# Kernel optimization log

Measured on AMD Instinct MI355X. Metric: run time of the kernel, lower is better.

## Reference

```python
import jax, jax.numpy as jnp
import numpy as np

N_NODES = 50000
N_EDGES = 800000
D = 128
N_LAYERS = 3
EPS = 1e-5  # torch LayerNorm default


def _gcn_conv(x, src, dst, dinv, W, b):
    # PyG GCNConv: h = x @ W; out[i] = sum_{(s->i)} dinv[s]*dinv[i]*h[s] + dinv[i]^2*h[i] + b
    h = x @ W
    norm = dinv[src] * dinv[dst]                      # [E]
    msgs = h[src] * norm[:, None]                     # [E, D] gather
    agg = jax.ops.segment_sum(msgs, dst, num_segments=N_NODES)  # scatter-add
    agg = agg + h * (dinv * dinv)[:, None]            # self-loop term
    return agg + b


def _layer_norm(x, gamma, beta):
    mu = jnp.mean(x, axis=-1, keepdims=True)
    var = jnp.mean(jnp.square(x - mu), axis=-1, keepdims=True)
    return (x - mu) * jax.lax.rsqrt(var + EPS) * gamma + beta


def setup_inputs() -> dict:
    key = jax.random.key(0)
    ks = jax.random.split(key, 4)
    x = jax.random.normal(ks[0], (N_NODES, D), dtype=jnp.float32)
    edge_index = jax.random.randint(ks[1], (2, N_EDGES), 0, N_NODES, dtype=jnp.int64)
    Ws = jax.random.normal(ks[2], (N_LAYERS, D, D), dtype=jnp.float32) * (1.0 / np.sqrt(D))
    bs = jnp.zeros((N_LAYERS, D), dtype=jnp.float32)
    gammas = jnp.ones((N_LAYERS, D), dtype=jnp.float32)
    betas = jnp.zeros((N_LAYERS, D), dtype=jnp.float32)
    return {"x": x, "edge_index": edge_index, "Ws": Ws, "bs": bs,
            "gammas": gammas, "betas": betas}


def reference(x, edge_index, Ws, bs, gammas, betas):
    src, dst = edge_index[0], edge_index[1]
    # GCN symmetric normalization with self-loops: deg[i] = in-degree(i) + 1
    deg = jnp.zeros((N_NODES,), dtype=x.dtype).at[dst].add(1.0) + 1.0
    dinv = jax.lax.rsqrt(deg)
    h = x
    for i in range(N_LAYERS):
        x_new = _gcn_conv(h, src, dst, dinv, Ws[i], bs[i])
        x_new = _layer_norm(x_new, gammas[i], betas[i])
        x_new = jax.nn.relu(x_new)  # dropout is identity in eval mode
        h = h + x_new if i > 0 else x_new
    return h
```

## Files before the change

kernel.cpp:

```cpp
#include <hip/hip_runtime.h>
#include <hip/hip_bf16.h>

#define NN 50000
#define NE 800000
#define DD 128
#define NB 196
#define NSB 49
#define PH (64 * NB)
#define FS 1024
#define NSL 782
#define HHB NSL
#define QB 3125
#define WB 192
#define LG 3125
#define LN_EPS 1e-5f

typedef __bf16 bf16x8 __attribute__((ext_vector_type(8)));
typedef float f32x4 __attribute__((ext_vector_type(4)));

__device__ inline ushort f2bf_bits(float f) {
    union { __hip_bfloat16 h; ushort u; } c;
    c.h = __float2bfloat16(f);
    return c.u;
}

__device__ inline void accum_q16(float* acc, uint4 v, float ww) {
    uint q0 = v.x, q1 = v.y, q2 = v.z, q3 = v.w;
    acc[0]  = fmaf(ww, (float)(char)(q0), acc[0]);
    acc[1]  = fmaf(ww, (float)(char)(q0 >> 8), acc[1]);
    acc[2]  = fmaf(ww, (float)(char)(q0 >> 16), acc[2]);
    acc[3]  = fmaf(ww, (float)(char)(q0 >> 24), acc[3]);
    acc[4]  = fmaf(ww, (float)(char)(q1), acc[4]);
    acc[5]  = fmaf(ww, (float)(char)(q1 >> 8), acc[5]);
    acc[6]  = fmaf(ww, (float)(char)(q1 >> 16), acc[6]);
    acc[7]  = fmaf(ww, (float)(char)(q1 >> 24), acc[7]);
    acc[8]  = fmaf(ww, (float)(char)(q2), acc[8]);
    acc[9]  = fmaf(ww, (float)(char)(q2 >> 8), acc[9]);
    acc[10] = fmaf(ww, (float)(char)(q2 >> 16), acc[10]);
    acc[11] = fmaf(ww, (float)(char)(q2 >> 24), acc[11]);
    acc[12] = fmaf(ww, (float)(char)(q3), acc[12]);
    acc[13] = fmaf(ww, (float)(char)(q3 >> 8), acc[13]);
    acc[14] = fmaf(ww, (float)(char)(q3 >> 16), acc[14]);
    acc[15] = fmaf(ww, (float)(char)(q3 >> 24), acc[15]);
}

__global__ void hist_cast_kernel(const int* __restrict__ dst, int* __restrict__ counts,
                                 int* __restrict__ rank, const float* __restrict__ x,
                                 uint2* __restrict__ qf0, float* __restrict__ sc0,
                                 const float* __restrict__ W, ushort* __restrict__ Wt) {
    int b = blockIdx.x;
    if (b < HHB) {
        int base = b * FS;
#pragma unroll 4
        for (int i = threadIdx.x; i < FS; i += 256) {
            int e = base + i;
            if (e < NE) rank[e] = atomicAdd(&counts[dst[e]], 1);
        }
    } else if (b < HHB + QB) {
        int bb = b - HHB;
        int group = threadIdx.x >> 4, t = threadIdx.x & 15;
        int node = bb * 16 + group;
        const float4* xr = (const float4*)(x + (size_t)node * DD + t * 8);
        float4 v0 = xr[0], v1 = xr[1];
        float vals[8] = {v0.x, v0.y, v0.z, v0.w, v1.x, v1.y, v1.z, v1.w};
        float am = 0.f;
#pragma unroll
        for (int i = 0; i < 8; ++i) am = fmaxf(am, fabsf(vals[i]));
#pragma unroll
        for (int off = 1; off <= 8; off <<= 1) am = fmaxf(am, __shfl_xor(am, off, 64));
        float inv = 127.f / fmaxf(am, 1e-20f);
        uint lo = 0, hi = 0;
#pragma unroll
        for (int i = 0; i < 4; ++i) {
            int q = __float2int_rn(vals[i] * inv);
            lo |= ((uint)(q & 0xff)) << (8 * i);
        }
#pragma unroll
        for (int i = 0; i < 4; ++i) {
            int q = __float2int_rn(vals[4 + i] * inv);
            hi |= ((uint)(q & 0xff)) << (8 * i);
        }
        uint2 pk; pk.x = lo; pk.y = hi;
        qf0[node * 16 + t] = pk;
        if (t == 0) sc0[node] = am / 127.f;
    } else {
        int i = (b - HHB - QB) * 256 + threadIdx.x;
        int l = i >> 14, k = (i >> 7) & 127, n = i & 127;
        Wt[l * 16384 + n * 128 + k] = f2bf_bits(W[i]);
    }
}

__global__ __launch_bounds__(1024) void scan1024_blocks(int* __restrict__ data,
                                                        int* __restrict__ bsums) {
    __shared__ int ws[16];
    int gid = blockIdx.x * 1024 + threadIdx.x;
    int lane = threadIdx.x & 63, wid = threadIdx.x >> 6;
    int v = (gid < NN) ? data[gid] : 0;
    int x = v;
#pragma unroll
    for (int off = 1; off < 64; off <<= 1) {
        int t = __shfl_up(x, off, 64);
        if (lane >= off) x += t;
    }
    if (lane == 63) ws[wid] = x;
    __syncthreads();
    if (threadIdx.x == 0) {
        int run = 0;
        for (int i = 0; i < 16; ++i) { int t = ws[i]; ws[i] = run; run += t; }
        bsums[blockIdx.x] = run;
    }
    __syncthreads();
    if (gid < NN) data[gid] = x - v + ws[wid];
}

__global__ __launch_bounds__(1024) void scan_sums1024(int* __restrict__ bsums, int nb) {
    __shared__ int ws[16];
    int tid = threadIdx.x;
    int lane = tid & 63, wid = tid >> 6;
    int v = (tid < nb) ? bsums[tid] : 0;
    int x = v;
#pragma unroll
    for (int off = 1; off < 64; off <<= 1) {
        int t = __shfl_up(x, off, 64);
        if (lane >= off) x += t;
    }
    if (lane == 63) ws[wid] = x;
    __syncthreads();
    if (tid == 0) {
        int run = 0;
        for (int i = 0; i < 16; ++i) { int t = ws[i]; ws[i] = run; run += t; }
    }
    __syncthreads();
    if (tid < nb) bsums[tid] = x - v + ws[wid];
}

__global__ void finalize_kernel(const int* __restrict__ excl, const int* __restrict__ bsums,
                                int* __restrict__ row_ptr, float* __restrict__ dinv,
                                int* __restrict__ degarr, int* __restrict__ bh) {
    __shared__ int lh[64];
    if (threadIdx.x < 64) lh[threadIdx.x] = 0;
    __syncthreads();
    int d = blockIdx.x * 256 + threadIdx.x;
    if (d < NN) {
        int p0 = excl[d] + bsums[d >> 10];
        int nxt = (d == NN - 1) ? NE : excl[d + 1] + bsums[(d + 1) >> 10];
        int deg = nxt - p0;
        row_ptr[d] = p0;
        dinv[d] = rsqrtf((float)deg + 1.0f);
        degarr[d] = deg;
        atomicAdd(&lh[63 - min(deg, 63)], 1);
    }
    __syncthreads();
    if (threadIdx.x < 64) bh[threadIdx.x * NB + blockIdx.x] = lh[threadIdx.x];
    if (blockIdx.x == 0 && threadIdx.x == 0) row_ptr[NN] = NE;
}

__global__ __launch_bounds__(1024) void permscan_kernel(int* __restrict__ bh) {
    __shared__ int wsum[16];
    const int CH = 13;
    int tid = threadIdx.x;
    int base = tid * CH;
    int vals[CH];
    int s = 0;
#pragma unroll
    for (int i = 0; i < CH; ++i) {
        int idx = base + i;
        int v = (idx < PH) ? bh[idx] : 0;
        vals[i] = s;
        s += v;
    }
    int lane = tid & 63, wid = tid >> 6;
    int x = s;
#pragma unroll
    for (int off = 1; off < 64; off <<= 1) {
        int t = __shfl_up(x, off, 64);
        if (lane >= off) x += t;
    }
    if (lane == 63) wsum[wid] = x;
    __syncthreads();
    if (tid == 0) {
        int run = 0;
        for (int i = 0; i < 16; ++i) { int t = wsum[i]; wsum[i] = run; run += t; }
    }
    __syncthreads();
    int texcl = x - s + wsum[wid];
#pragma unroll
    for (int i = 0; i < CH; ++i) {
        int idx = base + i;
        if (idx < PH) bh[idx] = texcl + vals[i];
    }
}

__global__ void scatter_fill_kernel(const int* __restrict__ degarr, const int* __restrict__ bh,
                                    int* __restrict__ perm, const int* __restrict__ src,
                                    const int* __restrict__ dst, const int* __restrict__ excl,
                                    const int* __restrict__ bsums, const int* __restrict__ rank,
                                    const float* __restrict__ dinv, int2* __restrict__ edge2) {
    if (blockIdx.x < NB) {
        __shared__ int lh[64];
        __shared__ int lbase[64];
        if (threadIdx.x < 64) {
            lh[threadIdx.x] = 0;
            lbase[threadIdx.x] = bh[threadIdx.x * NB + blockIdx.x];
        }
        __syncthreads();
        int gid = blockIdx.x * 256 + threadIdx.x;
        if (gid < NN) {
            int b = 63 - min(degarr[gid], 63);
            int r = atomicAdd(&lh[b], 1);
            perm[lbase[b] + r] = gid;
        }
    } else {
        int bb = blockIdx.x - NB;
        if (bb == 0 && threadIdx.x < 8) {
            int2 z; z.x = 0; z.y = 0;
            edge2[NE + threadIdx.x] = z;
        }
        int base = bb * FS;
#pragma unroll 4
        for (int i = threadIdx.x; i < FS; i += 256) {
            int e = base + i;
            if (e < NE) {
                int d = dst[e];
                int s = src[e];
                int pos = excl[d] + bsums[d >> 10] + rank[e];
                int2 o;
                o.x = s;
                o.y = __float_as_int(dinv[s] * dinv[d]);
                edge2[pos] = o;
            }
        }
    }
}

template <bool RES, bool FINAL>
__global__ __launch_bounds__(128) void layer_kernel(
    const uint4* __restrict__ qin, const float* __restrict__ scin,
    const ushort* __restrict__ fin, const int* __restrict__ row_ptr,
    const int2* __restrict__ edge2, const int* __restrict__ perm,
    const float* __restrict__ dinv, const ushort* __restrict__ Wt,
    const float* __restrict__ bias, const float* __restrict__ gamma,
    const float* __restrict__ beta, ushort* __restrict__ fout, char* __restrict__ qfout,
    float* __restrict__ scout, float* __restrict__ out) {
    __shared__ uint4 sA[16 * 17];
    __shared__ int sNode[16];
    __shared__ float sLN1[2][16], sLN2[2][16];
    __shared__ float sMX[2][16];

    int tid = threadIdx.x;
    int wv = tid >> 6, lane = tid & 63;
    int grp = lane >> 3, ln = lane & 7;
    int arow = wv * 8 + grp;
    int slot = blockIdx.x * 16 + arow;
    int node = perm[slot];
    if (ln == 0) sNode[arow] = node;

    {
        int beg = row_ptr[node], deg = row_ptr[node + 1] - beg;
        int nbt = (deg + 7) >> 3;
        float acc[16] = {};

        uint4 qself = qin[node * 8 + ln];
        float wself = dinv[node];
        wself = wself * wself * scin[node];

        const int2* eb = edge2 + beg;
        int bsel = lane & 56;
        for (int b = 0; b < nbt; ++b) {
            int lim = deg - b * 8;
            int2 a = eb[b * 8 + ln];
            float wf = __int_as_float(a.y) * scin[a.x];
            int sj[8];
            float W8[8];
#pragma unroll
            for (int j = 0; j < 8; ++j) sj[j] = __shfl(a.x, bsel + j, 64);
#pragma unroll
            for (int j = 0; j < 8; ++j) W8[j] = __shfl(wf, bsel + j, 64);
            uint4 Q[8];
#pragma unroll
            for (int j = 0; j < 8; ++j) Q[j] = qin[sj[j] * 8 + ln];
#pragma unroll
            for (int j = 0; j < 8; ++j) accum_q16(acc, Q[j], (j < lim) ? W8[j] : 0.f);
        }
        accum_q16(acc, qself, wself);

        union { ushort us[16]; uint4 u[2]; } pk;
#pragma unroll
        for (int i = 0; i < 16; ++i) pk.us[i] = f2bf_bits(acc[i]);
        sA[arow * 17 + 2 * ln] = pk.u[0];
        sA[arow * 17 + 2 * ln + 1] = pk.u[1];
    }
    __syncthreads();

    int q4 = lane >> 4, m = lane & 15;
    f32x4 c0 = (f32x4){0.f, 0.f, 0.f, 0.f};
    f32x4 c1 = c0, c2 = c0, c3 = c0;
    int ncb = 64 * wv;
#pragma unroll
    for (int kk = 0; kk < 4; ++kk) {
        bf16x8 af = *(const bf16x8*)&sA[m * 17 + kk * 4 + q4];
        const ushort* wb = Wt + (size_t)(ncb + m) * DD + kk * 32 + q4 * 8;
        c0 = __builtin_amdgcn_mfma_f32_16x16x32_bf16(af, *(const bf16x8*)(wb), c0, 0, 0, 0);
        c1 = __builtin_amdgcn_mfma_f32_16x16x32_bf16(af, *(const bf16x8*)(wb + 16 * DD), c1, 0, 0, 0);
        c2 = __builtin_amdgcn_mfma_f32_16x16x32_bf16(af, *(const bf16x8*)(wb + 32 * DD), c2, 0, 0, 0);
        c3 = __builtin_amdgcn_mfma_f32_16x16x32_bf16(af, *(const bf16x8*)(wb + 48 * DD), c3, 0, 0, 0);
    }

    float bb0 = bias[ncb + m], bb1 = bias[ncb + 16 + m];
    float bb2 = bias[ncb + 32 + m], bb3 = bias[ncb + 48 + m];
    float s1[4], s2[4];
#pragma unroll
    for (int r = 0; r < 4; ++r) {
        float v0 = c0[r] + bb0, v1 = c1[r] + bb1, v2 = c2[r] + bb2, v3 = c3[r] + bb3;
        c0[r] = v0; c1[r] = v1; c2[r] = v2; c3[r] = v3;
        s1[r] = (v0 + v1) + (v2 + v3);
        s2[r] = (v0 * v0 + v1 * v1) + (v2 * v2 + v3 * v3);
    }
#pragma unroll
    for (int off = 1; off <= 8; off <<= 1) {
#pragma unroll
        for (int r = 0; r < 4; ++r) {
            s1[r] += __shfl_xor(s1[r], off, 64);
            s2[r] += __shfl_xor(s2[r], off, 64);
        }
    }
    if (m == 0) {
#pragma unroll
        for (int r = 0; r < 4; ++r) {
            sLN1[wv][q4 * 4 + r] = s1[r];
            sLN2[wv][q4 * 4 + r] = s2[r];
        }
    }
    __syncthreads();
    float ga0 = gamma[ncb + m], ga1 = gamma[ncb + 16 + m];
    float ga2 = gamma[ncb + 32 + m], ga3 = gamma[ncb + 48 + m];
    float be0 = beta[ncb + m], be1 = beta[ncb + 16 + m];
    float be2 = beta[ncb + 32 + m], be3 = beta[ncb + 48 + m];
    float o0v[4], o1v[4], o2v[4], o3v[4], rmax[4];
#pragma unroll
    for (int r = 0; r < 4; ++r) {
        int row = q4 * 4 + r;
        float S1 = sLN1[0][row] + sLN1[1][row];
        float S2 = sLN2[0][row] + sLN2[1][row];
        float mu = S1 * (1.f / 128.f);
        float var = S2 * (1.f / 128.f) - mu * mu;
        float rstd = rsqrtf(var + LN_EPS);
        int nd = sNode[row];
        size_t rb = (size_t)nd * DD;
        float o0 = fmaxf((c0[r] - mu) * rstd * ga0 + be0, 0.f);
        float o1 = fmaxf((c1[r] - mu) * rstd * ga1 + be1, 0.f);
        float o2 = fmaxf((c2[r] - mu) * rstd * ga2 + be2, 0.f);
        float o3 = fmaxf((c3[r] - mu) * rstd * ga3 + be3, 0.f);
        if (RES) {
            o0 += __uint_as_float(((uint)fin[rb + ncb + m]) << 16);
            o1 += __uint_as_float(((uint)fin[rb + ncb + 16 + m]) << 16);
            o2 += __uint_as_float(((uint)fin[rb + ncb + 32 + m]) << 16);
            o3 += __uint_as_float(((uint)fin[rb + ncb + 48 + m]) << 16);
        }
        if (FINAL) {
            out[rb + ncb + m] = o0;
            out[rb + ncb + 16 + m] = o1;
            out[rb + ncb + 32 + m] = o2;
            out[rb + ncb + 48 + m] = o3;
        } else {
            fout[rb + ncb + m] = f2bf_bits(o0);
            fout[rb + ncb + 16 + m] = f2bf_bits(o1);
            fout[rb + ncb + 32 + m] = f2bf_bits(o2);
            fout[rb + ncb + 48 + m] = f2bf_bits(o3);
            o0v[r] = o0; o1v[r] = o1; o2v[r] = o2; o3v[r] = o3;
            rmax[r] = fmaxf(fmaxf(o0, o1), fmaxf(o2, o3));
        }
    }
    if (!FINAL) {
#pragma unroll
        for (int off = 1; off <= 8; off <<= 1) {
#pragma unroll
            for (int r = 0; r < 4; ++r) rmax[r] = fmaxf(rmax[r], __shfl_xor(rmax[r], off, 64));
        }
        if (m == 0) {
#pragma unroll
            for (int r = 0; r < 4; ++r) sMX[wv][q4 * 4 + r] = rmax[r];
        }
        __syncthreads();
#pragma unroll
        for (int r = 0; r < 4; ++r) {
            int row = q4 * 4 + r;
            float M = fmaxf(sMX[0][row], sMX[1][row]);
            float inv = 127.f / fmaxf(M, 1e-20f);
            int nd = sNode[row];
            if (wv == 0 && m == 0) scout[nd] = M / 127.f;
            size_t rb = (size_t)nd * DD;
            int q0 = min(__float2int_rn(o0v[r] * inv), 127);
            int q1 = min(__float2int_rn(o1v[r] * inv), 127);
            int q2 = min(__float2int_rn(o2v[r] * inv), 127);
            int q3 = min(__float2int_rn(o3v[r] * inv), 127);
            qfout[rb + ncb + m] = (char)q0;
            qfout[rb + ncb + 16 + m] = (char)q1;
            qfout[rb + ncb + 32 + m] = (char)q2;
            qfout[rb + ncb + 48 + m] = (char)q3;
        }
    }
}


extern "C" void kernel_launch(void* const* d_in, const int* in_sizes, int n_in,
                              void* d_out, int out_size, void* d_ws, size_t ws_size,
                              hipStream_t stream) {
    const float* x = (const float*)d_in[0];
    const int* edge = (const int*)d_in[1];
    const float* Ws = (const float*)d_in[2];
    const float* bs = (const float*)d_in[3];
    const float* gs = (const float*)d_in[4];
    const float* bes = (const float*)d_in[5];
    float* out = (float*)d_out;
    const int* src = edge;
    const int* dst = edge + NE;

    char* p = (char*)d_ws;
    int* counts = (int*)p;      p += (size_t)NN * 4;
    int* bsums = (int*)p;       p += 1024 * 4;
    int* row_ptr = (int*)p;     p += (size_t)(NN + 4) * 4;
    int* rank = (int*)p;        p += (size_t)NE * 4;
    float* dinv = (float*)p;    p += (size_t)NN * 4;
    int* degarr = (int*)p;      p += (size_t)NN * 4;
    int* bh = (int*)p;          p += (size_t)PH * 4;
    int* perm = (int*)p;        p += (size_t)NN * 4;
    int2* edge2 = (int2*)p;     p += (size_t)(NE + 8) * 8;
    ushort* fb0 = (ushort*)p;   p += (size_t)NN * DD * 2;
    ushort* fb1 = (ushort*)p;   p += (size_t)NN * DD * 2;
    char* qf0 = (char*)p;       p += (size_t)NN * DD;
    char* qf1 = (char*)p;       p += (size_t)NN * DD;
    float* sc0 = (float*)p;     p += (size_t)NN * 4;
    float* sc1 = (float*)p;     p += (size_t)NN * 4;
    ushort* Wt = (ushort*)p;    p += (size_t)3 * DD * DD * 2;

    hipMemsetAsync(counts, 0, (size_t)NN * 4, stream);
    hist_cast_kernel<<<HHB + QB + WB, 256, 0, stream>>>(dst, counts, rank, x,
                                                        (uint2*)qf0, sc0, Ws, Wt);
    scan1024_blocks<<<NSB, 1024, 0, stream>>>(counts, bsums);
    scan_sums1024<<<1, 1024, 0, stream>>>(bsums, NSB);
    finalize_kernel<<<NB, 256, 0, stream>>>(counts, bsums, row_ptr, dinv, degarr, bh);
    permscan_kernel<<<1, 1024, 0, stream>>>(bh);
    scatter_fill_kernel<<<NB + NSL, 256, 0, stream>>>(degarr, bh, perm, src, dst, counts,
                                                      bsums, rank, dinv, edge2);

    layer_kernel<false, false><<<LG, 128, 0, stream>>>(
        (const uint4*)qf0, sc0, fb0, row_ptr, edge2, perm, dinv, Wt, bs, gs, bes,
        fb1, qf1, sc1, out);
    layer_kernel<true, false><<<LG, 128, 0, stream>>>(
        (const uint4*)qf1, sc1, fb1, row_ptr, edge2, perm, dinv, Wt + 16384, bs + DD, gs + DD,
        bes + DD, fb0, qf0, sc0, out);
    layer_kernel<true, true><<<LG, 128, 0, stream>>>(
        (const uint4*)qf0, sc0, fb0, row_ptr, edge2, perm, dinv, Wt + 32768, bs + 2 * DD,
        gs + 2 * DD, bes + 2 * DD, fb1, qf1, sc1, out);
}
```

Measured before the change: 283.4 us.

## Fold single-block scans into last-block-done tails and double edge chunk size

The separate single-block kernels that scanned the block sums and the degree-bucket histogram are removed. Their work now runs in the tail of the preceding kernel, in whichever block finishes last according to an atomic counter with threadfences. This saves two kernel launches and their serialization gaps. Edge-processing blocks also handle 2048 edges each with a fully unrolled loop, so fewer blocks are launched, at the cost of less parallelism and a single-block serial tail that now runs with 256 threads and 49 elements each.

Measured after the change: 286.5 us. About the same (+1.1%).

```diff
diff --git a/kernel.cpp b/kernel.cpp
--- a/kernel.cpp
+++ b/kernel.cpp
@@ -7,8 +7,8 @@
 #define NB 196
 #define NSB 49
 #define PH (64 * NB)
-#define FS 1024
-#define NSL 782
+#define FS 2048
+#define NSL 391
 #define HHB NSL
 #define QB 3125
 #define WB 192
@@ -51,9 +51,9 @@
     int b = blockIdx.x;
     if (b < HHB) {
         int base = b * FS;
-#pragma unroll 4
-        for (int i = threadIdx.x; i < FS; i += 256) {
-            int e = base + i;
+#pragma unroll
+        for (int k = 0; k < 8; ++k) {
+            int e = base + k * 256 + threadIdx.x;
             if (e < NE) rank[e] = atomicAdd(&counts[dst[e]], 1);
         }
     } else if (b < HHB + QB) {
@@ -91,8 +91,11 @@
 }
 
 __global__ __launch_bounds__(1024) void scan1024_blocks(int* __restrict__ data,
-                                                        int* __restrict__ bsums) {
+                                                        int* __restrict__ bsums,
+                                                        int* __restrict__ done) {
     __shared__ int ws[16];
+    __shared__ int ws2[16];
+    __shared__ int isLast;
     int gid = blockIdx.x * 1024 + threadIdx.x;
     int lane = threadIdx.x & 63, wid = threadIdx.x >> 6;
     int v = (gid < NN) ? data[gid] : 0;
@@ -111,33 +114,38 @@
     }
     __syncthreads();
     if (gid < NN) data[gid] = x - v + ws[wid];
-}
-
-__global__ __launch_bounds__(1024) void scan_sums1024(int* __restrict__ bsums, int nb) {
-    __shared__ int ws[16];
+    if (threadIdx.x == 0) {
+        __threadfence();
+        isLast = (atomicAdd(done, 1) == NSB - 1);
+    }
+    __syncthreads();
+    if (!isLast) return;
+    __threadfence();
     int tid = threadIdx.x;
-    int lane = tid & 63, wid = tid >> 6;
-    int v = (tid < nb) ? bsums[tid] : 0;
-    int x = v;
+    int v2 = (tid < NSB) ? bsums[tid] : 0;
+    int x2 = v2;
 #pragma unroll
     for (int off = 1; off < 64; off <<= 1) {
-        int t = __shfl_up(x, off, 64);
-        if (lane >= off) x += t;
-    }
-    if (lane == 63) ws[wid] = x;
+        int t = __shfl_up(x2, off, 64);
+        if (lane >= off) x2 += t;
+    }
+    if (lane == 63) ws2[wid] = x2;
     __syncthreads();
     if (tid == 0) {
         int run = 0;
-        for (int i = 0; i < 16; ++i) { int t = ws[i]; ws[i] = run; run += t; }
-    }
-    __syncthreads();
-    if (tid < nb) bsums[tid] = x - v + ws[wid];
+        for (int i = 0; i < 16; ++i) { int t = ws2[i]; ws2[i] = run; run += t; }
+    }
+    __syncthreads();
+    if (tid < NSB) bsums[tid] = x2 - v2 + ws2[wid];
 }
 
 __global__ void finalize_kernel(const int* __restrict__ excl, const int* __restrict__ bsums,
                                 int* __restrict__ row_ptr, float* __restrict__ dinv,
-                                int* __restrict__ degarr, int* __restrict__ bh) {
+                                int* __restrict__ degarr, int* __restrict__ bh,
+                                int* __restrict__ done) {
     __shared__ int lh[64];
+    __shared__ int wsum[4];
+    __shared__ int isLast;
     if (threadIdx.x < 64) lh[threadIdx.x] = 0;
     __syncthreads();
     int d = blockIdx.x * 256 + threadIdx.x;
@@ -153,19 +161,21 @@
     __syncthreads();
     if (threadIdx.x < 64) bh[threadIdx.x * NB + blockIdx.x] = lh[threadIdx.x];
     if (blockIdx.x == 0 && threadIdx.x == 0) row_ptr[NN] = NE;
-}
-
-__global__ __launch_bounds__(1024) void permscan_kernel(int* __restrict__ bh) {
-    __shared__ int wsum[16];
-    const int CH = 13;
+    if (threadIdx.x == 0) {
+        __threadfence();
+        isLast = (atomicAdd(done, 1) == NB - 1);
+    }
+    __syncthreads();
+    if (!isLast) return;
+    __threadfence();
+    const int CH = 49;
     int tid = threadIdx.x;
     int base = tid * CH;
     int vals[CH];
     int s = 0;
 #pragma unroll
     for (int i = 0; i < CH; ++i) {
-        int idx = base + i;
-        int v = (idx < PH) ? bh[idx] : 0;
+        int v = bh[base + i];
         vals[i] = s;
         s += v;
     }
@@ -180,15 +190,12 @@
     __syncthreads();
     if (tid == 0) {
         int run = 0;
-        for (int i = 0; i < 16; ++i) { int t = wsum[i]; wsum[i] = run; run += t; }
+        for (int i = 0; i < 4; ++i) { int t = wsum[i]; wsum[i] = run; run += t; }
     }
     __syncthreads();
     int texcl = x - s + wsum[wid];
 #pragma unroll
-    for (int i = 0; i < CH; ++i) {
-        int idx = base + i;
-        if (idx < PH) bh[idx] = texcl + vals[i];
-    }
+    for (int i = 0; i < CH; ++i) bh[base + i] = texcl + vals[i];
 }
 
 __global__ void scatter_fill_kernel(const int* __restrict__ degarr, const int* __restrict__ bh,
@@ -217,9 +224,9 @@
             edge2[NE + threadIdx.x] = z;
         }
         int base = bb * FS;
-#pragma unroll 4
-        for (int i = threadIdx.x; i < FS; i += 256) {
-            int e = base + i;
+#pragma unroll
+        for (int k = 0; k < 8; ++k) {
+            int e = base + k * 256 + threadIdx.x;
             if (e < NE) {
                 int d = dst[e];
                 int s = src[e];
@@ -418,6 +425,7 @@
 
     char* p = (char*)d_ws;
     int* counts = (int*)p;      p += (size_t)NN * 4;
+    int* done = (int*)p;        p += 4 * 4;
     int* bsums = (int*)p;       p += 1024 * 4;
     int* row_ptr = (int*)p;     p += (size_t)(NN + 4) * 4;
     int* rank = (int*)p;        p += (size_t)NE * 4;
@@ -434,13 +442,12 @@
     float* sc1 = (float*)p;     p += (size_t)NN * 4;
     ushort* Wt = (ushort*)p;    p += (size_t)3 * DD * DD * 2;
 
-    hipMemsetAsync(counts, 0, (size_t)NN * 4, stream);
+    hipMemsetAsync(counts, 0, (size_t)(NN + 4) * 4, stream);
     hist_cast_kernel<<<HHB + QB + WB, 256, 0, stream>>>(dst, counts, rank, x,
                                                         (uint2*)qf0, sc0, Ws, Wt);
-    scan1024_blocks<<<NSB, 1024, 0, stream>>>(counts, bsums);
-    scan_sums1024<<<1, 1024, 0, stream>>>(bsums, NSB);
-    finalize_kernel<<<NB, 256, 0, stream>>>(counts, bsums, row_ptr, dinv, degarr, bh);
-    permscan_kernel<<<1, 1024, 0, stream>>>(bh);
+    scan1024_blocks<<<NSB, 1024, 0, stream>>>(counts, bsums, done);
+    finalize_kernel<<<NB, 256, 0, stream>>>(counts, bsums, row_ptr, dinv, degarr, bh,
+                                            done + 1);
     scatter_fill_kernel<<<NB + NSL, 256, 0, stream>>>(degarr, bh, perm, src, dst, counts,
                                                       bsums, rank, dinv, edge2);
 
```

## Split each node's edge gather across two lane groups with 256-thread blocks

Applied to the files above, without the earlier changes.

The layer kernel now launches 256 threads per 16-node block, so two 8-lane groups share each node's edge list and each sums half of the edge batches. The second group's partial sums pass through shared memory and are added before bf16 packing. In the MFMA stage each of the four waves computes 32 output columns instead of 64, and the LayerNorm and max reductions combine across four waves. The aim is more parallelism and latency hiding in the gather, at the cost of an extra barrier, extra shared memory and idle lanes on low-degree nodes.

Result: slower. 343.5 us (+21.2%).

```diff
diff --git a/kernel.cpp b/kernel.cpp
--- a/kernel.cpp
+++ b/kernel.cpp
@@ -234,7 +234,7 @@
 }
 
 template <bool RES, bool FINAL>
-__global__ __launch_bounds__(128) void layer_kernel(
+__global__ __launch_bounds__(256, 8) void layer_kernel(
     const uint4* __restrict__ qin, const float* __restrict__ scin,
     const ushort* __restrict__ fin, const int* __restrict__ row_ptr,
     const int2* __restrict__ edge2, const int* __restrict__ perm,
@@ -243,30 +243,39 @@
     const float* __restrict__ beta, ushort* __restrict__ fout, char* __restrict__ qfout,
     float* __restrict__ scout, float* __restrict__ out) {
     __shared__ uint4 sA[16 * 17];
+    __shared__ float pB[16][132];
     __shared__ int sNode[16];
-    __shared__ float sLN1[2][16], sLN2[2][16];
-    __shared__ float sMX[2][16];
+    __shared__ float sLN1[4][16], sLN2[4][16];
+    __shared__ float sMX[4][16];
 
     int tid = threadIdx.x;
     int wv = tid >> 6, lane = tid & 63;
-    int grp = lane >> 3, ln = lane & 7;
-    int arow = wv * 8 + grp;
-    int slot = blockIdx.x * 16 + arow;
+    int grp8 = lane >> 3, ln = lane & 7;
+    int gg = wv * 8 + grp8;
+    int nslot = gg >> 1, half = gg & 1;
+    int slot = blockIdx.x * 16 + nslot;
     int node = perm[slot];
-    if (ln == 0) sNode[arow] = node;
+    if (ln == 0 && half == 0) sNode[nslot] = node;
 
     {
         int beg = row_ptr[node], deg = row_ptr[node + 1] - beg;
         int nbt = (deg + 7) >> 3;
+        int nb2 = (nbt + 1) >> 1;
+        int bA = half ? nb2 : 0;
+        int bZ = half ? nbt : nb2;
         float acc[16] = {};
 
-        uint4 qself = qin[node * 8 + ln];
-        float wself = dinv[node];
-        wself = wself * wself * scin[node];
+        uint4 qself;
+        float wself = 0.f;
+        if (half == 0) {
+            qself = qin[node * 8 + ln];
+            float di = dinv[node];
+            wself = di * di * scin[node];
+        }
 
         const int2* eb = edge2 + beg;
         int bsel = lane & 56;
-        for (int b = 0; b < nbt; ++b) {
+        for (int b = bA; b < bZ; ++b) {
             int lim = deg - b * 8;
             int2 a = eb[b * 8 + ln];
             float wf = __int_as_float(a.y) * scin[a.x];
@@ -282,39 +291,48 @@
 #pragma unroll
             for (int j = 0; j < 8; ++j) accum_q16(acc, Q[j], (j < lim) ? W8[j] : 0.f);
         }
-        accum_q16(acc, qself, wself);
-
-        union { ushort us[16]; uint4 u[2]; } pk;
-#pragma unroll
-        for (int i = 0; i < 16; ++i) pk.us[i] = f2bf_bits(acc[i]);
-        sA[arow * 17 + 2 * ln] = pk.u[0];
-        sA[arow * 17 + 2 * ln + 1] = pk.u[1];
-    }
-    __syncthreads();
-
-    int q4 = lane >> 4, m = lane & 15;
+
+        if (half == 1) {
+            float4* d4 = (float4*)&pB[nslot][ln * 16];
+            d4[0] = (float4){acc[0], acc[1], acc[2], acc[3]};
+            d4[1] = (float4){acc[4], acc[5], acc[6], acc[7]};
+            d4[2] = (float4){acc[8], acc[9], acc[10], acc[11]};
+            d4[3] = (float4){acc[12], acc[13], acc[14], acc[15]};
+        }
+        __syncthreads();
+        if (half == 0) {
+            accum_q16(acc, qself, wself);
+            const float* pb = &pB[nslot][ln * 16];
+            union { ushort us[16]; uint4 u[2]; } pk;
+#pragma unroll
+            for (int i = 0; i < 16; ++i) pk.us[i] = f2bf_bits(acc[i] + pb[i]);
+            sA[nslot * 17 + 2 * ln] = pk.u[0];
+            sA[nslot * 17 + 2 * ln + 1] = pk.u[1];
+        }
+    }
+    __syncthreads();
+
+    int q = lane >> 4, m = lane & 15;
     f32x4 c0 = (f32x4){0.f, 0.f, 0.f, 0.f};
-    f32x4 c1 = c0, c2 = c0, c3 = c0;
-    int ncb = 64 * wv;
+    f32x4 c1 = (f32x4){0.f, 0.f, 0.f, 0.f};
+    int n0 = 16 * (2 * wv), n1 = 16 * (2 * wv + 1);
 #pragma unroll
     for (int kk = 0; kk < 4; ++kk) {
-        bf16x8 af = *(const bf16x8*)&sA[m * 17 + kk * 4 + q4];
-        const ushort* wb = Wt + (size_t)(ncb + m) * DD + kk * 32 + q4 * 8;
-        c0 = __builtin_amdgcn_mfma_f32_16x16x32_bf16(af, *(const bf16x8*)(wb), c0, 0, 0, 0);
-        c1 = __builtin_amdgcn_mfma_f32_16x16x32_bf16(af, *(const bf16x8*)(wb + 16 * DD), c1, 0, 0, 0);
-        c2 = __builtin_amdgcn_mfma_f32_16x16x32_bf16(af, *(const bf16x8*)(wb + 32 * DD), c2, 0, 0, 0);
-        c3 = __builtin_amdgcn_mfma_f32_16x16x32_bf16(af, *(const bf16x8*)(wb + 48 * DD), c3, 0, 0, 0);
-    }
-
-    float bb0 = bias[ncb + m], bb1 = bias[ncb + 16 + m];
-    float bb2 = bias[ncb + 32 + m], bb3 = bias[ncb + 48 + m];
+        bf16x8 af = *(const bf16x8*)&sA[m * 17 + kk * 4 + q];
+        bf16x8 b0 = *(const bf16x8*)(Wt + (n0 + m) * DD + kk * 32 + q * 8);
+        bf16x8 b1 = *(const bf16x8*)(Wt + (n1 + m) * DD + kk * 32 + q * 8);
+        c0 = __builtin_amdgcn_mfma_f32_16x16x32_bf16(af, b0, c0, 0, 0, 0);
+        c1 = __builtin_amdgcn_mfma_f32_16x16x32_bf16(af, b1, c1, 0, 0, 0);
+    }
+
+    float bb0 = bias[n0 + m], bb1 = bias[n1 + m];
     float s1[4], s2[4];
 #pragma unroll
     for (int r = 0; r < 4; ++r) {
-        float v0 = c0[r] + bb0, v1 = c1[r] + bb1, v2 = c2[r] + bb2, v3 = c3[r] + bb3;
-        c0[r] = v0; c1[r] = v1; c2[r] = v2; c3[r] = v3;
-        s1[r] = (v0 + v1) + (v2 + v3);
-        s2[r] = (v0 * v0 + v1 * v1) + (v2 * v2 + v3 * v3);
+        float v0 = c0[r] + bb0, v1 = c1[r] + bb1;
+        c0[r] = v0; c1[r] = v1;
+        s1[r] = v0 + v1;
+        s2[r] = v0 * v0 + v1 * v1;
     }
 #pragma unroll
     for (int off = 1; off <= 8; off <<= 1) {
@@ -327,21 +345,19 @@
     if (m == 0) {
 #pragma unroll
         for (int r = 0; r < 4; ++r) {
-            sLN1[wv][q4 * 4 + r] = s1[r];
-            sLN2[wv][q4 * 4 + r] = s2[r];
-        }
-    }
-    __syncthreads();
-    float ga0 = gamma[ncb + m], ga1 = gamma[ncb + 16 + m];
-    float ga2 = gamma[ncb + 32 + m], ga3 = gamma[ncb + 48 + m];
-    float be0 = beta[ncb + m], be1 = beta[ncb + 16 + m];
-    float be2 = beta[ncb + 32 + m], be3 = beta[ncb + 48 + m];
-    float o0v[4], o1v[4], o2v[4], o3v[4], rmax[4];
+            sLN1[wv][q * 4 + r] = s1[r];
+            sLN2[wv][q * 4 + r] = s2[r];
+        }
+    }
+    __syncthreads();
+    float ga0 = gamma[n0 + m], ga1 = gamma[n1 + m];
+    float be0 = beta[n0 + m], be1 = beta[n1 + m];
+    float o0v[4], o1v[4], rmax[4];
 #pragma unroll
     for (int r = 0; r < 4; ++r) {
-        int row = q4 * 4 + r;
-        float S1 = sLN1[0][row] + sLN1[1][row];
-        float S2 = sLN2[0][row] + sLN2[1][row];
+        int row = q * 4 + r;
+        float S1 = sLN1[0][row] + sLN1[1][row] + sLN1[2][row] + sLN1[3][row];
+        float S2 = sLN2[0][row] + sLN2[1][row] + sLN2[2][row] + sLN2[3][row];
         float mu = S1 * (1.f / 128.f);
         float var = S2 * (1.f / 128.f) - mu * mu;
         float rstd = rsqrtf(var + LN_EPS);
@@ -349,26 +365,18 @@
         size_t rb = (size_t)nd * DD;
         float o0 = fmaxf((c0[r] - mu) * rstd * ga0 + be0, 0.f);
         float o1 = fmaxf((c1[r] - mu) * rstd * ga1 + be1, 0.f);
-        float o2 = fmaxf((c2[r] - mu) * rstd * ga2 + be2, 0.f);
-        float o3 = fmaxf((c3[r] - mu) * rstd * ga3 + be3, 0.f);
         if (RES) {
-            o0 += __uint_as_float(((uint)fin[rb + ncb + m]) << 16);
-            o1 += __uint_as_float(((uint)fin[rb + ncb + 16 + m]) << 16);
-            o2 += __uint_as_float(((uint)fin[rb + ncb + 32 + m]) << 16);
-            o3 += __uint_as_float(((uint)fin[rb + ncb + 48 + m]) << 16);
+            o0 += __uint_as_float(((uint)fin[rb + n0 + m]) << 16);
+            o1 += __uint_as_float(((uint)fin[rb + n1 + m]) << 16);
         }
         if (FINAL) {
-            out[rb + ncb + m] = o0;
-            out[rb + ncb + 16 + m] = o1;
-            out[rb + ncb + 32 + m] = o2;
-            out[rb + ncb + 48 + m] = o3;
+            out[rb + n0 + m] = o0;
+            out[rb + n1 + m] = o1;
         } else {
-            fout[rb + ncb + m] = f2bf_bits(o0);
-            fout[rb + ncb + 16 + m] = f2bf_bits(o1);
-            fout[rb + ncb + 32 + m] = f2bf_bits(o2);
-            fout[rb + ncb + 48 + m] = f2bf_bits(o3);
-            o0v[r] = o0; o1v[r] = o1; o2v[r] = o2; o3v[r] = o3;
-            rmax[r] = fmaxf(fmaxf(o0, o1), fmaxf(o2, o3));
+            fout[rb + n0 + m] = f2bf_bits(o0);
+            fout[rb + n1 + m] = f2bf_bits(o1);
+            o0v[r] = o0; o1v[r] = o1;
+            rmax[r] = fmaxf(o0, o1);
         }
     }
     if (!FINAL) {
@@ -379,25 +387,21 @@
         }
         if (m == 0) {
 #pragma unroll
-            for (int r = 0; r < 4; ++r) sMX[wv][q4 * 4 + r] = rmax[r];
+            for (int r = 0; r < 4; ++r) sMX[wv][q * 4 + r] = rmax[r];
         }
         __syncthreads();
 #pragma unroll
         for (int r = 0; r < 4; ++r) {
-            int row = q4 * 4 + r;
-            float M = fmaxf(sMX[0][row], sMX[1][row]);
+            int row = q * 4 + r;
+            float M = fmaxf(fmaxf(sMX[0][row], sMX[1][row]), fmaxf(sMX[2][row], sMX[3][row]));
             float inv = 127.f / fmaxf(M, 1e-20f);
             int nd = sNode[row];
             if (wv == 0 && m == 0) scout[nd] = M / 127.f;
             size_t rb = (size_t)nd * DD;
             int q0 = min(__float2int_rn(o0v[r] * inv), 127);
             int q1 = min(__float2int_rn(o1v[r] * inv), 127);
-            int q2 = min(__float2int_rn(o2v[r] * inv), 127);
-            int q3 = min(__float2int_rn(o3v[r] * inv), 127);
-            qfout[rb + ncb + m] = (char)q0;
-            qfout[rb + ncb + 16 + m] = (char)q1;
-            qfout[rb + ncb + 32 + m] = (char)q2;
-            qfout[rb + ncb + 48 + m] = (char)q3;
+            qfout[rb + n0 + m] = (char)q0;
+            qfout[rb + n1 + m] = (char)q1;
         }
     }
 }
@@ -444,13 +448,13 @@
     scatter_fill_kernel<<<NB + NSL, 256, 0, stream>>>(degarr, bh, perm, src, dst, counts,
                                                       bsums, rank, dinv, edge2);
 
-    layer_kernel<false, false><<<LG, 128, 0, stream>>>(
+    layer_kernel<false, false><<<LG, 256, 0, stream>>>(
         (const uint4*)qf0, sc0, fb0, row_ptr, edge2, perm, dinv, Wt, bs, gs, bes,
         fb1, qf1, sc1, out);
-    layer_kernel<true, false><<<LG, 128, 0, stream>>>(
+    layer_kernel<true, false><<<LG, 256, 0, stream>>>(
         (const uint4*)qf1, sc1, fb1, row_ptr, edge2, perm, dinv, Wt + 16384, bs + DD, gs + DD,
         bes + DD, fb0, qf0, sc0, out);
-    layer_kernel<true, true><<<LG, 128, 0, stream>>>(
+    layer_kernel<true, true><<<LG, 256, 0, stream>>>(
         (const uint4*)qf0, sc0, fb0, row_ptr, edge2, perm, dinv, Wt + 32768, bs + 2 * DD,
         gs + 2 * DD, bes + 2 * DD, fb1, qf1, sc1, out);
 }
```
